# Kernel optimization log

Measured on AMD Instinct MI355X. Metric: run time of the kernel, lower is better.

Reference implementation:

```python
import jax, jax.numpy as jnp
import numpy as np

N_QUBITS = 10
EMBED_DIM = 512
FFN_DIM = 2048
DIM = 2 ** N_QUBITS


def _apply_rx(state, theta, wire):
    # state: (N, 2^n) complex64; theta: scalar or (N,)
    N = state.shape[0]
    hi = 2 ** wire                      # dims before the wire axis (wire 0 = MSB)
    lo = 2 ** (N_QUBITS - 1 - wire)
    s = state.reshape(N, hi, 2, lo)
    th = jnp.asarray(theta, jnp.float32).reshape(-1, 1, 1)  # (N,1,1) or (1,1,1)
    c = jnp.cos(th / 2).astype(jnp.complex64)
    ms = (-1j * jnp.sin(th / 2)).astype(jnp.complex64)
    s0, s1 = s[:, :, 0, :], s[:, :, 1, :]
    out = jnp.stack([c * s0 + ms * s1, ms * s0 + c * s1], axis=2)
    return out.reshape(N, DIM)


def _apply_cnot(state, ctrl, tgt):
    N = state.shape[0]
    s = state.reshape((N,) + (2,) * N_QUBITS)
    s0 = jax.lax.index_in_dim(s, 0, axis=ctrl + 1, keepdims=True)
    s1 = jax.lax.index_in_dim(s, 1, axis=ctrl + 1, keepdims=True)
    s1 = jnp.flip(s1, axis=tgt + 1)  # X on target where control == 1
    return jnp.concatenate([s0, s1], axis=ctrl + 1).reshape(N, DIM)


def _pauliz_signs():
    idx = np.arange(DIM)
    bits = (idx[:, None] >> (N_QUBITS - 1 - np.arange(N_QUBITS))[None, :]) & 1
    return jnp.asarray(1.0 - 2.0 * bits, jnp.float32)  # (2^n, n)


def _quantum_layer(tokens, rx_params):
    # tokens: (N, embed_dim); uses first n_qubits features as encoder angles
    N = tokens.shape[0]
    state = jnp.zeros((N, DIM), jnp.complex64).at[:, 0].set(1.0)
    for w in range(N_QUBITS):                    # encoder: RX(x_w) on wire w
        state = _apply_rx(state, tokens[:, w], w)
    for w in range(N_QUBITS):                    # trainable RX per wire
        state = _apply_rx(state, rx_params[w], w)
    for w in range(N_QUBITS - 1):                # CNOT chain
        state = _apply_cnot(state, w, w + 1)
    state = _apply_cnot(state, N_QUBITS - 1, 0)  # wrap-around CNOT
    probs = state.real ** 2 + state.imag ** 2    # (N, 2^n)
    return probs @ _pauliz_signs()               # (N, n_qubits) <Z_w>


def setup_inputs() -> dict:
    key = jax.random.key(0)
    ks = jax.random.split(key, 6)
    x = jax.random.normal(ks[0], (16, 1024, EMBED_DIM), jnp.float32)
    rx_params = jax.random.normal(ks[1], (N_QUBITS,), jnp.float32)
    lim1 = 1.0 / np.sqrt(N_QUBITS)
    w1 = jax.random.uniform(ks[2], (FFN_DIM, N_QUBITS), jnp.float32, -lim1, lim1)
    b1 = jax.random.uniform(ks[3], (FFN_DIM,), jnp.float32, -lim1, lim1)
    lim2 = 1.0 / np.sqrt(FFN_DIM)
    w2 = jax.random.uniform(ks[4], (EMBED_DIM, FFN_DIM), jnp.float32, -lim2, lim2)
    b2 = jax.random.uniform(ks[5], (EMBED_DIM,), jnp.float32, -lim2, lim2)
    return {"x": x, "rx_params": rx_params, "w1": w1, "b1": b1, "w2": w2, "b2": b2}


def reference(x, rx_params, w1, b1, w2, b2):
    B, S, _ = x.shape
    q_out = _quantum_layer(x.reshape(B * S, EMBED_DIM), rx_params)
    q_out = q_out.reshape(B, S, N_QUBITS)
    h = jax.nn.relu(q_out @ w1.T + b1)           # dropout is identity in eval
    return h @ w2.T + b2
```

## Files before the change

kernel.cpp:

```cpp
#include <hip/hip_runtime.h>
#include <hip/hip_bf16.h>
#include <math.h>


typedef __attribute__((ext_vector_type(8))) short short8;
typedef __attribute__((ext_vector_type(8))) unsigned short ushort8;
typedef __attribute__((ext_vector_type(4))) float fx4;

constexpr int EDIM = 512;
constexpr int FDIM = 2048;
constexpr int NQ   = 10;
constexpr int BK   = 64;
constexpr int NCH  = FDIM / BK;

__device__ __forceinline__ ushort f2bf(float f) {
    union { float f; unsigned u; } v; v.f = f;
    unsigned u = v.u + 0x7FFFu + ((v.u >> 16) & 1u);
    return (ushort)(u >> 16);
}
__device__ __forceinline__ unsigned bits2(__hip_bfloat162 h) {
    union { __hip_bfloat162 h; unsigned u; } v; v.h = h; return v.u;
}
__device__ __forceinline__ void gload_lds16(const void* g, void* l) {
    __builtin_amdgcn_global_load_lds(
        (const __attribute__((address_space(1))) void*)g,
        (__attribute__((address_space(3))) void*)l, 16, 0, 0);
}

__global__ void prep(const float* __restrict__ w2, ushort* __restrict__ w2b) {
    int gid = blockIdx.x * blockDim.x + threadIdx.x;
    int np  = gridDim.x * blockDim.x;
    for (int i = gid; i < EDIM * FDIM / 4; i += np) {
        float4 v = ((const float4*)w2)[i];
        ushort4 o; o.x = f2bf(v.x); o.y = f2bf(v.y); o.z = f2bf(v.z); o.w = f2bf(v.w);
        ((ushort4*)w2b)[i] = o;
    }
}

__global__ __launch_bounds__(256, 2) void gemm1(
    const float* __restrict__ x, const float* __restrict__ rx,
    const float* __restrict__ w1, const float* __restrict__ b1,
    ushort* __restrict__ h, int m_base)
{
    __shared__ float qs[32][NQ];
    const int tid = threadIdx.x;
    const int m0  = m_base + blockIdx.x * 32;

    if (tid < 32) {
        const float* xr = x + (size_t)(m0 + tid) * EDIM;
        float c[NQ], q[NQ];
        #pragma unroll
        for (int w = 0; w < NQ; ++w) c[w] = cosf(xr[w] + rx[w]);
        float p0 = c[1];
        #pragma unroll
        for (int w = 2; w < NQ; ++w) p0 *= c[w];
        q[0] = p0;
        float p = c[0];
        #pragma unroll
        for (int w = 1; w < NQ; ++w) { p *= c[w]; q[w] = p; }
        #pragma unroll
        for (int w = 0; w < NQ; ++w) qs[tid][w] = q[w];
    }
    __syncthreads();

    float wv[80];
    {
        const float4* wp = (const float4*)(w1 + (size_t)tid * 80);
        #pragma unroll
        for (int u = 0; u < 20; ++u) ((float4*)wv)[u] = wp[u];
    }
    float bv[8];
    {
        float4 a = *(const float4*)(b1 + tid * 8);
        float4 b = *(const float4*)(b1 + tid * 8 + 4);
        bv[0]=a.x; bv[1]=a.y; bv[2]=a.z; bv[3]=a.w;
        bv[4]=b.x; bv[5]=b.y; bv[6]=b.z; bv[7]=b.w;
    }
    ushort* hrow = h + (size_t)m0 * FDIM + tid * 8;

    for (int m = 0; m < 32; ++m) {
        float qv[NQ];
        #pragma unroll
        for (int w = 0; w < NQ; ++w) qv[w] = qs[m][w];
        float a[8];
        #pragma unroll
        for (int r = 0; r < 8; ++r) a[r] = bv[r];
        #pragma unroll
        for (int w = 0; w < NQ; ++w)
            #pragma unroll
            for (int r = 0; r < 8; ++r)
                a[r] = fmaf(qv[w], wv[r * 10 + w], a[r]);
        ushort8 o;
        #pragma unroll
        for (int r = 0; r < 4; ++r) {
            unsigned p = bits2(__float22bfloat162_rn(
                make_float2(fmaxf(a[2*r], 0.f), fmaxf(a[2*r+1], 0.f))));
            o[2*r]   = (ushort)(p & 0xFFFFu);
            o[2*r+1] = (ushort)(p >> 16);
        }
        *(ushort8*)(hrow + (size_t)m * FDIM) = o;
    }
}

__global__ __launch_bounds__(256, 2) void gemm2(
    const ushort* __restrict__ h,
    const ushort* __restrict__ w2b,
    const float* __restrict__ b2,
    float* __restrict__ out, int m_base)
{
    __shared__ ushort As[128 * BK];
    __shared__ ushort Bs[128 * BK];

    const int tid  = threadIdx.x;
    const int bm   = blockIdx.x;
    const int bn   = blockIdx.y;
    const int m0   = m_base + bm * 128, n0 = bn * 128;
    const int wave = tid >> 6, lane = tid & 63;
    const int quad = lane >> 4, l16 = lane & 15;
    const int wm   = wave >> 1, wn = wave & 1;

    const int srow0 = tid >> 3;
    const int sbs   = tid & 7;
    const ushort* gA[4]; const ushort* gB[4];
    #pragma unroll
    for (int u = 0; u < 4; ++u) {
        int row = u * 32 + srow0;
        int bl  = sbs ^ (row & 7);
        gA[u] = h   + (size_t)(m0 + row) * FDIM + bl * 8;
        gB[u] = w2b + (size_t)(n0 + row) * FDIM + bl * 8;
    }
    const int ldst = wave * 512;

    const int swz = l16 & 7;
    int aro[4], bro[4];
    #pragma unroll
    for (int t = 0; t < 4; ++t) {
        aro[t] = (wm * 64 + t * 16 + l16) * BK;
        bro[t] = (wn * 64 + t * 16 + l16) * BK;
    }

    fx4 acc[4][4];
    #pragma unroll
    for (int a = 0; a < 4; ++a)
        #pragma unroll
        for (int b = 0; b < 4; ++b) acc[a][b] = fx4{0.f, 0.f, 0.f, 0.f};

    for (int i = 0; i < NCH; ++i) {
        #pragma unroll
        for (int u = 0; u < 4; ++u) {
            gload_lds16(gA[u], &As[u * 2048 + ldst]);
            gload_lds16(gB[u], &Bs[u * 2048 + ldst]);
            gA[u] += BK; gB[u] += BK;
        }
        __syncthreads();

        short8 af[4][2], bf[4][2];
        #pragma unroll
        for (int t = 0; t < 4; ++t)
            #pragma unroll
            for (int hf = 0; hf < 2; ++hf) {
                const int blk = (hf * 4 + quad) ^ swz;
                af[t][hf] = *(const short8*)&As[aro[t] + blk * 8];
                bf[t][hf] = *(const short8*)&Bs[bro[t] + blk * 8];
            }

        #pragma unroll
        for (int hf = 0; hf < 2; ++hf)
            #pragma unroll
            for (int mt = 0; mt < 4; ++mt)
                #pragma unroll
                for (int nt = 0; nt < 4; ++nt)
                    acc[mt][nt] = __builtin_amdgcn_mfma_f32_16x16x32_bf16(
                        af[mt][hf], bf[nt][hf], acc[mt][nt], 0, 0, 0);
        __syncthreads();
    }

    float bb[4];
    #pragma unroll
    for (int nt = 0; nt < 4; ++nt) bb[nt] = b2[n0 + wn * 64 + nt * 16 + l16];
    #pragma unroll
    for (int mt = 0; mt < 4; ++mt) {
        const int mbase = m0 + wm * 64 + mt * 16 + quad * 4;
        #pragma unroll
        for (int nt = 0; nt < 4; ++nt) {
            const int n = n0 + wn * 64 + nt * 16 + l16;
            #pragma unroll
            for (int r = 0; r < 4; ++r)
                out[(size_t)(mbase + r) * EDIM + n] = acc[mt][nt][r] + bb[nt];
        }
    }
}

extern "C" void kernel_launch(void* const* d_in, const int* in_sizes, int n_in,
                              void* d_out, int out_size, void* d_ws, size_t ws_size,
                              hipStream_t stream) {
    const float* x  = (const float*)d_in[0];
    const float* rx = (const float*)d_in[1];
    const float* w1 = (const float*)d_in[2];
    const float* b1 = (const float*)d_in[3];
    const float* w2 = (const float*)d_in[4];
    const float* b2 = (const float*)d_in[5];
    float* out = (float*)d_out;

    const int M = in_sizes[0] / EDIM;

    const size_t w2bytes = (size_t)EDIM * FDIM * 2;
    ushort* w2b = (ushort*)d_ws;
    ushort* h   = (ushort*)((char*)d_ws + w2bytes);

    int Ms = M;
    {
        size_t avail = (ws_size > w2bytes) ? ws_size - w2bytes : 0;
        int cap = (int)(avail / ((size_t)FDIM * 2));
        cap &= ~127;
        if (cap < 128) cap = 128;
        if (Ms > cap) Ms = cap;
    }

    hipLaunchKernelGGL(prep, dim3(256), dim3(256), 0, stream, w2, w2b);

    for (int mb = 0; mb < M; mb += Ms) {
        int cur = (M - mb < Ms) ? (M - mb) : Ms;
        hipLaunchKernelGGL(gemm1, dim3(cur / 32), dim3(256), 0, stream,
                           x, rx, w1, b1, h, mb);
        hipLaunchKernelGGL(gemm2, dim3(cur / 128, 4), dim3(256), 0, stream,
                           h, w2b, b2, out, mb);
    }
}
```

Before: 140.4 us.

## Fuse FFN first layer into second GEMM via MFMA with split-bf16 operands

```diff
diff --git a/kernel.cpp b/kernel.cpp
--- a/kernel.cpp
+++ b/kernel.cpp
@@ -11,6 +11,8 @@
 constexpr int FDIM = 2048;
 constexpr int NQ   = 10;
 constexpr int BK   = 64;
+constexpr int BM   = 128;
+constexpr int BN   = 128;
 constexpr int NCH  = FDIM / BK;
 
 __device__ __forceinline__ ushort f2bf(float f) {
@@ -18,6 +20,9 @@
     unsigned u = v.u + 0x7FFFu + ((v.u >> 16) & 1u);
     return (ushort)(u >> 16);
 }
+__device__ __forceinline__ float bf2f(ushort u) {
+    union { unsigned u; float f; } v; v.u = (unsigned)u << 16; return v.f;
+}
 __device__ __forceinline__ unsigned bits2(__hip_bfloat162 h) {
     union { __hip_bfloat162 h; unsigned u; } v; v.h = h; return v.u;
 }
@@ -27,7 +32,9 @@
         (__attribute__((address_space(3))) void*)l, 16, 0, 0);
 }
 
-__global__ void prep(const float* __restrict__ w2, ushort* __restrict__ w2b) {
+__global__ void prep(const float* __restrict__ w2, const float* __restrict__ w1,
+                     const float* __restrict__ b1,
+                     ushort* __restrict__ w2b, ushort* __restrict__ w1t) {
     int gid = blockIdx.x * blockDim.x + threadIdx.x;
     int np  = gridDim.x * blockDim.x;
     for (int i = gid; i < EDIM * FDIM / 4; i += np) {
@@ -35,22 +42,48 @@
         ushort4 o; o.x = f2bf(v.x); o.y = f2bf(v.y); o.z = f2bf(v.z); o.w = f2bf(v.w);
         ((ushort4*)w2b)[i] = o;
     }
-}
-
-__global__ __launch_bounds__(256, 2) void gemm1(
+    for (int f = gid; f < FDIM; f += np) {
+        ushort zr[32];
+        #pragma unroll
+        for (int w = 0; w < NQ; ++w) {
+            float v  = w1[f * NQ + w];
+            ushort hb = f2bf(v);
+            ushort lb = f2bf(v - bf2f(hb));
+            zr[w] = hb; zr[10 + w] = hb; zr[20 + w] = lb;
+        }
+        float bv  = b1[f];
+        ushort bh = f2bf(bv);
+        zr[30] = bh; zr[31] = f2bf(bv - bf2f(bh));
+        #pragma unroll
+        for (int u = 0; u < 4; ++u)
+            *(ushort8*)&w1t[f * 32 + u * 8] = *(ushort8*)&zr[u * 8];
+    }
+}
+
+__global__ __launch_bounds__(256, 2) void fused(
     const float* __restrict__ x, const float* __restrict__ rx,
-    const float* __restrict__ w1, const float* __restrict__ b1,
-    ushort* __restrict__ h, int m_base)
+    const ushort* __restrict__ w1t,
+    const ushort* __restrict__ w2b,
+    const float* __restrict__ b2,
+    float* __restrict__ out)
 {
-    __shared__ float qs[32][NQ];
+    __shared__ __align__(16) ushort Zs[BM * 32];
+    __shared__ __align__(16) ushort As[2][BM * BK];
+    __shared__ __align__(16) ushort Bs[2][BN * BK];
+
     const int tid = threadIdx.x;
-    const int m0  = m_base + blockIdx.x * 32;
-
-    if (tid < 32) {
+    const int m0  = blockIdx.x * BM;
+    const int n0  = blockIdx.y * BN;
+
+    if (tid < BM) {
         const float* xr = x + (size_t)(m0 + tid) * EDIM;
+        float4 xa = *(const float4*)xr;
+        float4 xb = *(const float4*)(xr + 4);
+        float2 xc = *(const float2*)(xr + 8);
+        float xv[NQ] = {xa.x, xa.y, xa.z, xa.w, xb.x, xb.y, xb.z, xb.w, xc.x, xc.y};
         float c[NQ], q[NQ];
         #pragma unroll
-        for (int w = 0; w < NQ; ++w) c[w] = cosf(xr[w] + rx[w]);
+        for (int w = 0; w < NQ; ++w) c[w] = cosf(xv[w] + rx[w]);
         float p0 = c[1];
         #pragma unroll
         for (int w = 2; w < NQ; ++w) p0 *= c[w];
@@ -58,80 +91,43 @@
         float p = c[0];
         #pragma unroll
         for (int w = 1; w < NQ; ++w) { p *= c[w]; q[w] = p; }
-        #pragma unroll
-        for (int w = 0; w < NQ; ++w) qs[tid][w] = q[w];
+        ushort zr[32];
+        #pragma unroll
+        for (int w = 0; w < NQ; ++w) {
+            ushort hb = f2bf(q[w]);
+            ushort lb = f2bf(q[w] - bf2f(hb));
+            zr[w] = hb; zr[10 + w] = lb; zr[20 + w] = hb;
+        }
+        zr[30] = 0x3F80u; zr[31] = 0x3F80u;
+        #pragma unroll
+        for (int u = 0; u < 4; ++u)
+            *(ushort8*)&Zs[tid * 32 + u * 8] = *(ushort8*)&zr[u * 8];
     }
     __syncthreads();
 
-    float wv[80];
-    {
-        const float4* wp = (const float4*)(w1 + (size_t)tid * 80);
-        #pragma unroll
-        for (int u = 0; u < 20; ++u) ((float4*)wv)[u] = wp[u];
-    }
-    float bv[8];
-    {
-        float4 a = *(const float4*)(b1 + tid * 8);
-        float4 b = *(const float4*)(b1 + tid * 8 + 4);
-        bv[0]=a.x; bv[1]=a.y; bv[2]=a.z; bv[3]=a.w;
-        bv[4]=b.x; bv[5]=b.y; bv[6]=b.z; bv[7]=b.w;
-    }
-    ushort* hrow = h + (size_t)m0 * FDIM + tid * 8;
-
-    for (int m = 0; m < 32; ++m) {
-        float qv[NQ];
-        #pragma unroll
-        for (int w = 0; w < NQ; ++w) qv[w] = qs[m][w];
-        float a[8];
-        #pragma unroll
-        for (int r = 0; r < 8; ++r) a[r] = bv[r];
-        #pragma unroll
-        for (int w = 0; w < NQ; ++w)
-            #pragma unroll
-            for (int r = 0; r < 8; ++r)
-                a[r] = fmaf(qv[w], wv[r * 10 + w], a[r]);
-        ushort8 o;
-        #pragma unroll
-        for (int r = 0; r < 4; ++r) {
-            unsigned p = bits2(__float22bfloat162_rn(
-                make_float2(fmaxf(a[2*r], 0.f), fmaxf(a[2*r+1], 0.f))));
-            o[2*r]   = (ushort)(p & 0xFFFFu);
-            o[2*r+1] = (ushort)(p >> 16);
-        }
-        *(ushort8*)(hrow + (size_t)m * FDIM) = o;
-    }
-}
-
-__global__ __launch_bounds__(256, 2) void gemm2(
-    const ushort* __restrict__ h,
-    const ushort* __restrict__ w2b,
-    const float* __restrict__ b2,
-    float* __restrict__ out, int m_base)
-{
-    __shared__ ushort As[128 * BK];
-    __shared__ ushort Bs[128 * BK];
-
-    const int tid  = threadIdx.x;
-    const int bm   = blockIdx.x;
-    const int bn   = blockIdx.y;
-    const int m0   = m_base + bm * 128, n0 = bn * 128;
     const int wave = tid >> 6, lane = tid & 63;
     const int quad = lane >> 4, l16 = lane & 15;
     const int wm   = wave >> 1, wn = wave & 1;
+    const int swz  = l16 & 7;
+
+    const int hm0 = (wave & 1) * 64;
+    const int hf0 = (wave >> 1) * 32;
+    short8 zf[4];
+    #pragma unroll
+    for (int mi = 0; mi < 4; ++mi)
+        zf[mi] = *(const short8*)&Zs[(hm0 + mi * 16 + l16) * 32 + quad * 8];
 
     const int srow0 = tid >> 3;
     const int sbs   = tid & 7;
-    const ushort* gA[4]; const ushort* gB[4];
+    const ushort* gB[4];
     #pragma unroll
     for (int u = 0; u < 4; ++u) {
         int row = u * 32 + srow0;
         int bl  = sbs ^ (row & 7);
-        gA[u] = h   + (size_t)(m0 + row) * FDIM + bl * 8;
         gB[u] = w2b + (size_t)(n0 + row) * FDIM + bl * 8;
     }
     const int ldst = wave * 512;
 
-    const int swz = l16 & 7;
     int aro[4], bro[4];
     #pragma unroll
     for (int t = 0; t < 4; ++t) {
@@ -145,35 +141,78 @@
         #pragma unroll
         for (int b = 0; b < 4; ++b) acc[a][b] = fx4{0.f, 0.f, 0.f, 0.f};
 
-    for (int i = 0; i < NCH; ++i) {
-        #pragma unroll
-        for (int u = 0; u < 4; ++u) {
-            gload_lds16(gA[u], &As[u * 2048 + ldst]);
-            gload_lds16(gB[u], &Bs[u * 2048 + ldst]);
-            gA[u] += BK; gB[u] += BK;
-        }
+    short8 wfE[2], wfO[2];
+
+#define WLOAD(WF, CH) do { _Pragma("unroll") \
+    for (int fi = 0; fi < 2; ++fi) \
+        WF[fi] = *(const short8*)(w1t + ((CH) * 64 + hf0 + fi * 16 + l16) * 32 + quad * 8); \
+} while (0)
+
+#define STAGEB(BUF) do { _Pragma("unroll") \
+    for (int u = 0; u < 4; ++u) { gload_lds16(gB[u], &Bs[BUF][u * 2048 + ldst]); gB[u] += BK; } \
+} while (0)
+
+#define HPROD(BUF, WF) do { _Pragma("unroll") \
+    for (int mi = 0; mi < 4; ++mi) { \
+        const int hrow = hm0 + mi * 16 + l16; \
+        ushort* arow = &As[BUF][hrow * BK]; \
+        _Pragma("unroll") \
+        for (int fi = 0; fi < 2; ++fi) { \
+            fx4 hv = __builtin_amdgcn_mfma_f32_16x16x32_bf16( \
+                WF[fi], zf[mi], fx4{0.f, 0.f, 0.f, 0.f}, 0, 0, 0); \
+            unsigned ua = bits2(__float22bfloat162_rn( \
+                make_float2(fmaxf(hv[0], 0.f), fmaxf(hv[1], 0.f)))); \
+            unsigned ub = bits2(__float22bfloat162_rn( \
+                make_float2(fmaxf(hv[2], 0.f), fmaxf(hv[3], 0.f)))); \
+            const int blk = (hf0 >> 3) + fi * 2 + (quad >> 1); \
+            *(uint2*)&arow[((blk ^ swz) << 3) + ((quad & 1) << 2)] = make_uint2(ua, ub); \
+        } \
+    } \
+} while (0)
+
+#define COMPUTE(BUF) do { \
+    short8 af[4][2], bf[4][2]; \
+    _Pragma("unroll") \
+    for (int t = 0; t < 4; ++t) \
+        _Pragma("unroll") \
+        for (int hf = 0; hf < 2; ++hf) { \
+            const int blkb = (((hf * 4 + quad) ^ swz) << 3); \
+            af[t][hf] = *(const short8*)&As[BUF][aro[t] + blkb]; \
+            bf[t][hf] = *(const short8*)&Bs[BUF][bro[t] + blkb]; \
+        } \
+    _Pragma("unroll") \
+    for (int hf = 0; hf < 2; ++hf) \
+        _Pragma("unroll") \
+        for (int mt = 0; mt < 4; ++mt) \
+            _Pragma("unroll") \
+            for (int nt = 0; nt < 4; ++nt) \
+                acc[mt][nt] = __builtin_amdgcn_mfma_f32_16x16x32_bf16( \
+                    af[mt][hf], bf[nt][hf], acc[mt][nt], 0, 0, 0); \
+} while (0)
+
+    STAGEB(0);
+    WLOAD(wfE, 0);
+    HPROD(0, wfE);
+    WLOAD(wfO, 1);
+    __syncthreads();
+
+    for (int p = 0; p < 15; ++p) {
+        STAGEB(1); HPROD(1, wfO); WLOAD(wfE, 2 * p + 2);
+        COMPUTE(0);
         __syncthreads();
-
-        short8 af[4][2], bf[4][2];
-        #pragma unroll
-        for (int t = 0; t < 4; ++t)
-            #pragma unroll
-            for (int hf = 0; hf < 2; ++hf) {
-                const int blk = (hf * 4 + quad) ^ swz;
-                af[t][hf] = *(const short8*)&As[aro[t] + blk * 8];
-                bf[t][hf] = *(const short8*)&Bs[bro[t] + blk * 8];
-            }
-
-        #pragma unroll
-        for (int hf = 0; hf < 2; ++hf)
-            #pragma unroll
-            for (int mt = 0; mt < 4; ++mt)
-                #pragma unroll
-                for (int nt = 0; nt < 4; ++nt)
-                    acc[mt][nt] = __builtin_amdgcn_mfma_f32_16x16x32_bf16(
-                        af[mt][hf], bf[nt][hf], acc[mt][nt], 0, 0, 0);
+        STAGEB(0); HPROD(0, wfE); WLOAD(wfO, 2 * p + 3);
+        COMPUTE(1);
         __syncthreads();
     }
+    STAGEB(1); HPROD(1, wfO);
+    COMPUTE(0);
+    __syncthreads();
+    COMPUTE(1);
+
+#undef COMPUTE
+#undef HPROD
+#undef STAGEB
+#undef WLOAD
 
     float bb[4];
     #pragma unroll
@@ -204,26 +243,11 @@
 
     const int M = in_sizes[0] / EDIM;
 
-    const size_t w2bytes = (size_t)EDIM * FDIM * 2;
     ushort* w2b = (ushort*)d_ws;
-    ushort* h   = (ushort*)((char*)d_ws + w2bytes);
-
-    int Ms = M;
-    {
-        size_t avail = (ws_size > w2bytes) ? ws_size - w2bytes : 0;
-        int cap = (int)(avail / ((size_t)FDIM * 2));
-        cap &= ~127;
-        if (cap < 128) cap = 128;
-        if (Ms > cap) Ms = cap;
-    }
-
-    hipLaunchKernelGGL(prep, dim3(256), dim3(256), 0, stream, w2, w2b);
-
-    for (int mb = 0; mb < M; mb += Ms) {
-        int cur = (M - mb < Ms) ? (M - mb) : Ms;
-        hipLaunchKernelGGL(gemm1, dim3(cur / 32), dim3(256), 0, stream,
-                           x, rx, w1, b1, h, mb);
-        hipLaunchKernelGGL(gemm2, dim3(cur / 128, 4), dim3(256), 0, stream,
-                           h, w2b, b2, out, mb);
-    }
-}
+    ushort* w1t = (ushort*)((char*)d_ws + (size_t)EDIM * FDIM * 2);
+    (void)ws_size; (void)n_in; (void)out_size;
+
+    hipLaunchKernelGGL(prep, dim3(256), dim3(256), 0, stream, w2, w1, b1, w2b, w1t);
+    hipLaunchKernelGGL(fused, dim3(M / BM, EDIM / BN), dim3(256), 0, stream,
+                       x, rx, w1t, w2b, b2, out);
+}
```

New measurement: 138.6 us. No clear change (-1.2%).
